# Optimization experiments

Measured on AMD Instinct MI355X. Metric: run time of the kernel, lower is better.

The kernel has to match this reference:

```python
import jax, jax.numpy as jnp
import numpy as np

N_NODES = 100000
N_EDGES = 1600000
IN_F, HID_F, OUT_F = 128, 128, 64
BN_EPS = 1e-5


def _glorot(key, shape):
    lim = np.sqrt(6.0 / (shape[0] + shape[1]))
    return jax.random.uniform(key, shape, jnp.float32, -lim, lim)


def setup_inputs() -> dict:
    key = jax.random.key(0)
    ks = jax.random.split(key, 12)
    x = jax.random.normal(ks[0], (N_NODES, IN_F), jnp.float32)
    src = jax.random.randint(ks[1], (N_EDGES,), 0, N_NODES, jnp.int64)
    dst = jax.random.randint(ks[2], (N_EDGES,), 0, N_NODES, jnp.int64)
    dims = [(IN_F, HID_F), (HID_F, HID_F), (HID_F, OUT_F)]
    inp = {"x": x, "src": src, "dst": dst}
    for i, (di, do) in enumerate(dims):
        inp[f"w_self{i}"] = _glorot(ks[3 + 2 * i], (di, do))
        inp[f"w_neigh{i}"] = _glorot(ks[4 + 2 * i], (di, do))
        inp[f"b{i}"] = jnp.zeros((do,), jnp.float32)
    for i in range(2):  # BatchNorm1d(hid) after first two convs
        inp[f"gamma{i}"] = jnp.ones((HID_F,), jnp.float32)
        inp[f"beta{i}"] = jnp.zeros((HID_F,), jnp.float32)
    return inp


def _sage_conv(h, src, dst, w_self, w_neigh, b):
    # mean aggregation over incoming edges: gather src feats, segment-sum by dst
    deg = jax.ops.segment_sum(jnp.ones((src.shape[0],), h.dtype), dst, num_segments=N_NODES)
    agg = jax.ops.segment_sum(h[src], dst, num_segments=N_NODES)
    agg = agg / jnp.maximum(deg, 1.0)[:, None]
    return h @ w_self + agg @ w_neigh + b


def _batchnorm(h, gamma, beta):
    mu = jnp.mean(h, axis=0)
    var = jnp.var(h, axis=0)
    return (h - mu) * jax.lax.rsqrt(var + BN_EPS) * gamma + beta


def reference(x, src, dst, w_self0, w_neigh0, b0, gamma0, beta0,
              w_self1, w_neigh1, b1, gamma1, beta1, w_self2, w_neigh2, b2):
    h = _sage_conv(x, src, dst, w_self0, w_neigh0, b0)
    h = jax.nn.relu(_batchnorm(h, gamma0, beta0))
    h = _sage_conv(h, src, dst, w_self1, w_neigh1, b1)
    h = jax.nn.relu(_batchnorm(h, gamma1, beta1))
    h = _sage_conv(h, src, dst, w_self2, w_neigh2, b2)
    return jax.nn.log_softmax(h, axis=-1)
```

## Files before the change

### kernel.cpp

```cpp
#include <hip/hip_runtime.h>
#include <hip/hip_bf16.h>

typedef unsigned short u16;
typedef unsigned char  u8;
typedef unsigned int   u32;
typedef __attribute__((ext_vector_type(8))) short short8;
typedef __attribute__((ext_vector_type(4))) float floatx4;
typedef __attribute__((ext_vector_type(2))) float floatx2;

__device__ __forceinline__ float bits2f(u32 v){ float f; __builtin_memcpy(&f, &v, 4); return f; }
__device__ __forceinline__ u16 f2bf(float f){
    __hip_bfloat16 h = __float2bfloat16(f);
    u16 u; __builtin_memcpy(&u, &h, 2); return u;
}

__device__ __forceinline__ void gload_lds16(const void* g, void* l){
    __builtin_amdgcn_global_load_lds(
        (const __attribute__((address_space(1))) unsigned char*)g,
        (__attribute__((address_space(3))) unsigned char*)l, 16, 0, 0);
}


__global__ __launch_bounds__(256) void cvt_kernel(const float* __restrict__ in,
                                                  u16* __restrict__ out,
                                                  u32* __restrict__ out8, int total4){
    int i = blockIdx.x * 256 + threadIdx.x;
    if (i >= total4) return;
    float4 v = ((const float4*)in)[i];
    uint2 o;
    o.x = (u32)f2bf(v.x) | ((u32)f2bf(v.y) << 16);
    o.y = (u32)f2bf(v.z) | ((u32)f2bf(v.w) << 16);
    ((uint2*)out)[i] = o;
    u32 p8 = (u32)__builtin_amdgcn_cvt_pk_fp8_f32(v.x, v.y, 0, false);
    p8     = (u32)__builtin_amdgcn_cvt_pk_fp8_f32(v.z, v.w, (int)p8, true);
    out8[i] = p8;
}


__global__ __launch_bounds__(256) void cvt8a_kernel(const u16* __restrict__ in,
                                                    const float* __restrict__ cs,
                                                    uint2* __restrict__ out8, int total8){
    int i = blockIdx.x * 256 + threadIdx.x;
    if (i >= total8) return;
    const int c0 = (i & 15) * 8;
    uint4 v = ((const uint4*)in)[i];
    u32 w[4] = {v.x, v.y, v.z, v.w};
    float f[8];
    #pragma unroll
    for (int j = 0; j < 4; ++j){
        f[2*j]   = bits2f(w[j] << 16);
        f[2*j+1] = bits2f(w[j] & 0xffff0000u);
    }
    #pragma unroll
    for (int j = 0; j < 8; ++j)
        f[j] = fmaxf(fmaf(f[j], cs[256 + c0 + j], cs[384 + c0 + j]), 0.f);
    u32 lo = (u32)__builtin_amdgcn_cvt_pk_fp8_f32(f[0], f[1], 0, false);
    lo     = (u32)__builtin_amdgcn_cvt_pk_fp8_f32(f[2], f[3], (int)lo, true);
    u32 hi = (u32)__builtin_amdgcn_cvt_pk_fp8_f32(f[4], f[5], 0, false);
    hi     = (u32)__builtin_amdgcn_cvt_pk_fp8_f32(f[6], f[7], (int)hi, true);
    uint2 o; o.x = lo; o.y = hi;
    out8[i] = o;
}


__global__ __launch_bounds__(256) void bhist_kernel(const int* __restrict__ dst,
                                                    int* __restrict__ gbcnt, int E){
    __shared__ int bc[256];
    const int t = threadIdx.x;
    bc[t] = 0;
    __syncthreads();
    const int tile0 = blockIdx.x * 8192;
    const int cnt = min(8192, E - tile0);
    for (int j = t; j < cnt; j += 256) atomicAdd(&bc[dst[tile0 + j] >> 9], 1);
    __syncthreads();
    if (bc[t] > 0) atomicAdd(&gbcnt[t], bc[t]);
}

__global__ __launch_bounds__(256) void bscan_kernel(const int* __restrict__ gbcnt,
                                                    int* __restrict__ bbase,
                                                    int* __restrict__ bcur, int nbuk){
    __shared__ int ws[4];
    const int t = threadIdx.x, lane = t & 63, wv = t >> 6;
    int v = (t < nbuk) ? gbcnt[t] : 0;
    int s = v;
    for (int off = 1; off < 64; off <<= 1){
        int n = __shfl_up(s, off);
        if (lane >= off) s += n;
    }
    if (lane == 63) ws[wv] = s;
    __syncthreads();
    int woff = 0;
    for (int w = 0; w < wv; ++w) woff += ws[w];
    int excl = s + woff - v;
    if (t < nbuk){ bbase[t] = excl; bcur[t] = excl; }
}

#define BIN_TILE 8192
__global__ __launch_bounds__(256) void bin_kernel(const int* __restrict__ src,
                                                  const int* __restrict__ dst,
                                                  int* __restrict__ bcur,
                                                  u32* __restrict__ pairs, int E, int nbuk){
    __shared__ u32 hcnt[256], hexcl[256], hoff[256];
    __shared__ int gbase[256];
    __shared__ u32 stage[BIN_TILE];
    __shared__ unsigned char bkt[BIN_TILE];
    const int t = threadIdx.x;
    const int tile0 = blockIdx.x * BIN_TILE;
    const int cntE = min(BIN_TILE, E - tile0);

    hcnt[t] = 0;
    __syncthreads();
    for (int j = t; j < cntE; j += 256){
        int d = dst[tile0 + j];
        atomicAdd(&hcnt[d >> 9], 1u);
    }
    __syncthreads();
    if (t < 64){
        u32 a0 = hcnt[4*t], a1 = hcnt[4*t+1], a2 = hcnt[4*t+2], a3 = hcnt[4*t+3];
        u32 lsum = a0 + a1 + a2 + a3;
        u32 s = lsum;
        for (int off = 1; off < 64; off <<= 1){
            u32 n = __shfl_up(s, off);
            if (t >= off) s += n;
        }
        u32 base = s - lsum;
        hexcl[4*t]   = base;
        hexcl[4*t+1] = base + a0;
        hexcl[4*t+2] = base + a0 + a1;
        hexcl[4*t+3] = base + a0 + a1 + a2;
        hoff[4*t]   = base;
        hoff[4*t+1] = base + a0;
        hoff[4*t+2] = base + a0 + a1;
        hoff[4*t+3] = base + a0 + a1 + a2;
    }
    __syncthreads();
    if (t < nbuk && hcnt[t] > 0) gbase[t] = atomicAdd(&bcur[t], (int)hcnt[t]);
    for (int j = t; j < cntE; j += 256){
        int d = dst[tile0 + j];
        int s = src[tile0 + j];
        int b = d >> 9;
        u32 p = atomicAdd(&hoff[b], 1u);
        stage[p] = ((u32)s << 9) | (u32)(d & 511);
        bkt[p] = (unsigned char)b;
    }
    __syncthreads();
    for (int j = t; j < cntE; j += 256){
        int b = bkt[j];
        pairs[gbase[b] + (int)((u32)j - hexcl[b])] = stage[j];
    }
}

__global__ __launch_bounds__(256) void sort2_kernel(const u32* __restrict__ pairs,
                                                    const int* __restrict__ bbase,
                                                    int* __restrict__ indptr,
                                                    float* __restrict__ invdeg,
                                                    int* __restrict__ esrc,
                                                    int M, int E, int nbuk){
    __shared__ int ndeg[512];
    __shared__ int cur[512];
    __shared__ int wsI[4];
    const int b = blockIdx.x;
    const int node0 = b * 512;
    const int lo = bbase[b];
    const int hi = (b + 1 < nbuk) ? bbase[b + 1] : E;
    const int t = threadIdx.x, lane = t & 63, wv = t >> 6;

    ndeg[t] = 0; ndeg[t + 256] = 0;
    __syncthreads();
    for (int i = lo + t; i < hi; i += 256) atomicAdd(&ndeg[pairs[i] & 511], 1);
    __syncthreads();

    const int d0 = ndeg[2*t], d1 = ndeg[2*t + 1];
    const int p = d0 + d1;
    int s = p;
    for (int off = 1; off < 64; off <<= 1){
        int n = __shfl_up(s, off);
        if (lane >= off) s += n;
    }
    if (lane == 63) wsI[wv] = s;
    __syncthreads();
    int woff = 0;
    for (int w = 0; w < wv; ++w) woff += wsI[w];
    const int incl = s + woff;
    const int excl0 = incl - p;
    const int excl1 = excl0 + d0;

    const int n0 = node0 + 2*t, n1 = node0 + 2*t + 1;
    if (n0 < M){
        indptr[n0 + 1] = lo + excl0 + d0;
        invdeg[n0] = 1.0f / (float)max(d0, 1);
        cur[2*t] = lo + excl0;
    }
    if (n1 < M){
        indptr[n1 + 1] = lo + excl1 + d1;
        invdeg[n1] = 1.0f / (float)max(d1, 1);
        cur[2*t + 1] = lo + excl1;
    }
    if (b == 0 && t == 0) indptr[0] = 0;
    __syncthreads();
    for (int i = lo + t; i < hi; i += 256){
        u32 v = pairs[i];
        int pos = atomicAdd(&cur[v & 511], 1);
        esrc[pos] = (int)(v >> 9);
    }
}


__global__ void pack_kernel(const float* __restrict__ wself, const float* __restrict__ wneigh,
                            u16* __restrict__ bp, int N){
    int i = blockIdx.x * 256 + threadIdx.x;
    if (i >= N * 256) return;
    int n = i >> 8, k = i & 255;
    float v = (k < 128) ? wself[k * N + n] : wneigh[(k - 128) * N + n];
    bp[i] = f2bf(v);
}


__global__ __launch_bounds__(256) void agg_kernel(const u8* __restrict__ h8,
                                                  const int* __restrict__ indptr,
                                                  const int* __restrict__ esrc,
                                                  const float* __restrict__ invdeg,
                                                  u16* __restrict__ agg, int M){
    const int l8 = threadIdx.x & 7;
    const int n = (blockIdx.x * 256 + threadIdx.x) >> 3;
    if (n >= M) return;
    const int beg = indptr[n];
    const int end = indptr[n + 1];
    const float fs = invdeg[n];

    floatx2 acc[8];
    #pragma unroll
    for (int i = 0; i < 8; ++i){ acc[i].x = 0.f; acc[i].y = 0.f; }

    const u8* hb = h8 + l8 * 16;

    auto accum = [&](uint4 v){
        u32 w[4] = {v.x, v.y, v.z, v.w};
        #pragma unroll
        for (int j = 0; j < 4; ++j){
            acc[2*j]   += __builtin_amdgcn_cvt_pk_f32_fp8(w[j], false);
            acc[2*j+1] += __builtin_amdgcn_cvt_pk_f32_fp8(w[j], true);
        }
    };

    int e = beg;
    for (; e + 4 <= end; e += 4){
        const int i0 = esrc[e];
        const int i1 = esrc[e + 1];
        const int i2 = esrc[e + 2];
        const int i3 = esrc[e + 3];
        uint4 v0 = *(const uint4*)(hb + (size_t)i0 * 128);
        uint4 v1 = *(const uint4*)(hb + (size_t)i1 * 128);
        uint4 v2 = *(const uint4*)(hb + (size_t)i2 * 128);
        uint4 v3 = *(const uint4*)(hb + (size_t)i3 * 128);
        accum(v0); accum(v1); accum(v2); accum(v3);
    }
    for (; e < end; ++e){
        const int i0 = esrc[e];
        uint4 v0 = *(const uint4*)(hb + (size_t)i0 * 128);
        accum(v0);
    }

    u32 o[8];
    #pragma unroll
    for (int k = 0; k < 8; ++k)
        o[k] = (u32)f2bf(acc[k].x * fs) | ((u32)f2bf(acc[k].y * fs) << 16);
    uint4 w0 = {o[0], o[1], o[2], o[3]};
    uint4 w1 = {o[4], o[5], o[6], o[7]};
    *(uint4*)(agg + (size_t)n * 128 + l8 * 16)     = w0;
    *(uint4*)(agg + (size_t)n * 128 + l8 * 16 + 8) = w1;
}


template<int NTW, bool STATS, bool AFFA>
__global__ __launch_bounds__(256, 4) void gemm3_kernel(const u16* __restrict__ hA,
                                                       const u16* __restrict__ aggA,
                                                       const u16* __restrict__ Bp,
                                                       const float* __restrict__ bias,
                                                       const float* __restrict__ cs,
                                                       void* __restrict__ outPre,
                                                       float* __restrict__ partials,
                                                       int M, int T, int GBs){
    constexpr int N = NTW * 64;
    __shared__ __align__(16) u16 Abuf[3][4096];
    __shared__ __align__(16) char cbuf[2][4352];
    __shared__ float s_sc[128], s_sh[128];

    const int wave = threadIdx.x >> 6;
    const int lane = threadIdx.x & 63;
    const int m15 = lane & 15;
    const int quad = lane >> 4;
    const int colbase = wave * (NTW * 16);

    if (AFFA && threadIdx.x < 128){
        s_sc[threadIdx.x] = cs[256 + threadIdx.x];
        s_sh[threadIdx.x] = cs[384 + threadIdx.x];
    }
    __syncthreads();

    short8 breg[NTW][8];
    float bv[NTW];
    #pragma unroll
    for (int nt = 0; nt < NTW; ++nt){
        bv[nt] = bias[colbase + nt * 16 + m15];
        #pragma unroll
        for (int k0 = 0; k0 < 8; ++k0)
            breg[nt][k0] = *(const short8*)(Bp + (size_t)(colbase + nt * 16 + m15) * 256 + k0 * 32 + quad * 8);
    }

    float sS[NTW], sQ[NTW];
    #pragma unroll
    for (int nt = 0; nt < NTW; ++nt){ sS[nt] = 0.f; sQ[nt] = 0.f; }

    auto stage = [&](int bufIdx, int tile){
        const int srow = lane & 15, squad = lane >> 4;
        int arow = tile * 16 + srow;
        if (arow >= M) arow = M - 1;
        #pragma unroll
        for (int h = 0; h < 2; ++h){
            const int k0 = wave * 2 + h;
            const u16* base = (k0 < 4) ? hA : aggA;
            const u16* g = base + (size_t)arow * 128 + (k0 & 3) * 32 + squad * 8;
            gload_lds16(g, &Abuf[bufIdx][k0 * 512]);
        }
    };

    const int t0 = blockIdx.x;
    const int nIter = (T - 1 - t0) / GBs + 1;

    stage(0, t0);
    if (nIter > 1) stage(1, t0 + GBs);

    int t = t0;
    for (int it = 0; it < nIter; ++it){
        const int cur = it % 3;
        if (it + 2 < nIter) stage((it + 2) % 3, t + 2 * GBs);

        const int ahead = min(nIter - 1 - it, 2);
        if (ahead >= 2)      asm volatile("s_waitcnt vmcnt(4)" ::: "memory");
        else if (ahead == 1) asm volatile("s_waitcnt vmcnt(2)" ::: "memory");
        else                 asm volatile("s_waitcnt vmcnt(0)" ::: "memory");
        __builtin_amdgcn_s_barrier();
        __builtin_amdgcn_sched_barrier(0);

        floatx4 acc[NTW];
        #pragma unroll
        for (int nt = 0; nt < NTW; ++nt) acc[nt] = 0.0f;
        #pragma unroll
        for (int k0 = 0; k0 < 8; ++k0){
            short8 a = *(const short8*)&Abuf[cur][k0 * 512 + quad * 128 + m15 * 8];
            if (AFFA && k0 < 4){
                const int cb = k0 * 32 + quad * 8;
                #pragma unroll
                for (int j = 0; j < 8; ++j){
                    float f = bits2f(((u32)(u16)a[j]) << 16);
                    f = fmaxf(fmaf(f, s_sc[cb + j], s_sh[cb + j]), 0.f);
                    a[j] = (short)f2bf(f);
                }
            }
            #pragma unroll
            for (int nt = 0; nt < NTW; ++nt)
                acc[nt] = __builtin_amdgcn_mfma_f32_16x16x32_bf16(a, breg[nt][k0], acc[nt], 0, 0, 0);
        }

        char* cb = &cbuf[it & 1][0];
        const int r0 = quad * 4;
        #pragma unroll
        for (int nt = 0; nt < NTW; ++nt){
            const int col = colbase + nt * 16 + m15;
            #pragma unroll
            for (int r = 0; r < 4; ++r){
                float v = acc[nt][r] + bv[nt];
                if (STATS){
                    int row = t * 16 + r0 + r;
                    if (row < M){
                        sS[nt] += v;
                        sQ[nt] = fmaf(v, v, sQ[nt]);
                    }
                    ((u16*)cb)[(r0 + r) * 136 + col] = f2bf(v);
                } else {
                    ((float*)cb)[(r0 + r) * 68 + col] = v;
                }
            }
        }
        asm volatile("s_waitcnt lgkmcnt(0)" ::: "memory");
        __builtin_amdgcn_s_barrier();
        __builtin_amdgcn_sched_barrier(0);

        const int srow = threadIdx.x >> 4, seg = threadIdx.x & 15;
        const int grow = t * 16 + srow;
        if (grow < M){
            if (STATS){
                uint4 w = *(const uint4*)((const u16*)cb + srow * 136 + seg * 8);
                *(uint4*)((u16*)outPre + (size_t)grow * N + seg * 8) = w;
            } else {
                float4 w = *(const float4*)((const float*)cb + srow * 68 + seg * 4);
                *(float4*)((float*)outPre + (size_t)grow * N + seg * 4) = w;
            }
        }
        t += GBs;
    }

    if (STATS){
        #pragma unroll
        for (int nt = 0; nt < NTW; ++nt){
            float s = sS[nt], q = sQ[nt];
            s += __shfl_xor(s, 16);  s += __shfl_xor(s, 32);
            q += __shfl_xor(q, 16);  q += __shfl_xor(q, 32);
            if (quad == 0){
                const int c = colbase + nt * 16 + m15;
                partials[(size_t)blockIdx.x * 256 + c]       = s;
                partials[(size_t)blockIdx.x * 256 + 128 + c] = q;
            }
        }
    }
}


__global__ __launch_bounds__(256) void bnred_kernel(const float* __restrict__ partials,
                                                    float* __restrict__ cs, int nblk){
    const int t = threadIdx.x;
    float s = 0.f;
    for (int b = blockIdx.x; b < nblk; b += (int)gridDim.x)
        s += partials[(size_t)b * 256 + t];
    atomicAdd(&cs[t], s);
}

__global__ void bnfin_kernel(float* __restrict__ cs, const float* __restrict__ gamma,
                             const float* __restrict__ beta, float invM){
    int c = threadIdx.x;
    float mu  = cs[c] * invM;
    float var = fmaxf(cs[128 + c] * invM - mu * mu, 0.0f);
    float sc  = gamma[c] * rsqrtf(var + 1e-5f);
    cs[256 + c] = sc;
    cs[384 + c] = beta[c] - mu * sc;
}


__global__ __launch_bounds__(256) void lsm_kernel(const float* __restrict__ pre,
                                                  float* __restrict__ out, int M){
    const int wave = threadIdx.x >> 6;
    const int lane = threadIdx.x & 63;
    const int row = blockIdx.x * 4 + wave;
    if (row >= M) return;
    float v = pre[(size_t)row * 64 + lane];
    float m = v;
    #pragma unroll
    for (int o = 32; o; o >>= 1) m = fmaxf(m, __shfl_xor(m, o));
    float e = __expf(v - m);
    float s = e;
    #pragma unroll
    for (int o = 32; o; o >>= 1) s += __shfl_xor(s, o);
    out[(size_t)row * 64 + lane] = v - m - __logf(s);
}


extern "C" void kernel_launch(void* const* d_in, const int* in_sizes, int n_in,
                              void* d_out, int out_size, void* d_ws, size_t ws_size,
                              hipStream_t stream) {
    const float* x   = (const float*)d_in[0];
    const int*   src = (const int*)d_in[1];
    const int*   dst = (const int*)d_in[2];
    const float* wself[3]  = {(const float*)d_in[3], (const float*)d_in[6], (const float*)d_in[9]};
    const float* wneigh[3] = {(const float*)d_in[4], (const float*)d_in[7], (const float*)d_in[10]};
    const float* bias[3]   = {(const float*)d_in[5], (const float*)d_in[8], (const float*)d_in[11]};
    const float* gamma[2]  = {(const float*)d_in[12], (const float*)d_in[14]};
    const float* beta[2]   = {(const float*)d_in[13], (const float*)d_in[15]};

    const int M = in_sizes[0] / 128;
    const int E = in_sizes[1];
    const int NBUK = (M + 511) / 512;
    const int T = (M + 15) / 16;
    const int GB = 1024;

    char* ws = (char*)d_ws;
    size_t off = 0;
    auto alloc = [&](size_t bytes) -> void* {
        void* p = ws + off;
        off = (off + bytes + 511) & ~(size_t)511;
        return p;
    };
    int*   gbcnt  = (int*)alloc(256 * 4);
    int*   bbase  = (int*)alloc(256 * 4);
    int*   bcur   = (int*)alloc(256 * 4);
    int*   indptr = (int*)alloc((size_t)(M + 1) * 4);
    u32*   pairs  = (u32*)alloc((size_t)E * 4);
    int*   esrc   = (int*)alloc((size_t)E * 4);
    float* invdeg = (float*)alloc((size_t)M * 4);
    u16* bpack0 = (u16*)alloc(128 * 256 * 2);
    u16* bpack1 = (u16*)alloc(128 * 256 * 2);
    u16* bpack2 = (u16*)alloc(64 * 256 * 2);
    float* colstat0 = (float*)alloc(512 * 4);
    float* colstat1 = (float*)alloc(512 * 4);
    float* partials = (float*)alloc((size_t)GB * 256 * 4);
    u16*   hbuf   = (u16*)alloc((size_t)M * 128 * 2);
    u16*   aggbuf = (u16*)alloc((size_t)M * 128 * 2);
    u16*   preA   = (u16*)alloc((size_t)M * 128 * 2);
    u16*   preB   = (u16*)alloc((size_t)M * 128 * 2);
    float* preF   = (float*)alloc((size_t)M * 64 * 4);
    u8*    x8     = (u8*)alloc((size_t)M * 128);
    u8*    preA8  = (u8*)alloc((size_t)M * 128);
    u8*    preB8  = (u8*)alloc((size_t)M * 128);

    hipMemsetAsync(gbcnt, 0, 256 * 4, stream);
    bhist_kernel<<<(E + 8191) / 8192, 256, 0, stream>>>(dst, gbcnt, E);
    bscan_kernel<<<1, 256, 0, stream>>>(gbcnt, bbase, bcur, NBUK);
    bin_kernel<<<(E + BIN_TILE - 1) / BIN_TILE, 256, 0, stream>>>(src, dst, bcur, pairs, E, NBUK);
    sort2_kernel<<<NBUK, 256, 0, stream>>>(pairs, bbase, indptr, invdeg, esrc, M, E, NBUK);

    cvt_kernel<<<((M * 32) + 255) / 256, 256, 0, stream>>>(x, hbuf, (u32*)x8, M * 32);
    pack_kernel<<<(128 * 256 + 255) / 256, 256, 0, stream>>>(wself[0], wneigh[0], bpack0, 128);
    pack_kernel<<<(128 * 256 + 255) / 256, 256, 0, stream>>>(wself[1], wneigh[1], bpack1, 128);
    pack_kernel<<<(64 * 256 + 255) / 256, 256, 0, stream>>>(wself[2], wneigh[2], bpack2, 64);

    agg_kernel<<<(M + 31) / 32, 256, 0, stream>>>(x8, indptr, esrc, invdeg, aggbuf, M);
    gemm3_kernel<2, true, false><<<GB, 256, 0, stream>>>(hbuf, aggbuf, bpack0, bias[0], nullptr,
                                                         preA, partials, M, T, GB);
    hipMemsetAsync(colstat0, 0, 256 * 4, stream);
    bnred_kernel<<<32, 256, 0, stream>>>(partials, colstat0, GB);
    bnfin_kernel<<<1, 128, 0, stream>>>(colstat0, gamma[0], beta[0], 1.0f / (float)M);
    cvt8a_kernel<<<((M * 16) + 255) / 256, 256, 0, stream>>>(preA, colstat0, (uint2*)preA8, M * 16);

    agg_kernel<<<(M + 31) / 32, 256, 0, stream>>>(preA8, indptr, esrc, invdeg, aggbuf, M);
    gemm3_kernel<2, true, true><<<GB, 256, 0, stream>>>(preA, aggbuf, bpack1, bias[1], colstat0,
                                                        preB, partials, M, T, GB);
    hipMemsetAsync(colstat1, 0, 256 * 4, stream);
    bnred_kernel<<<32, 256, 0, stream>>>(partials, colstat1, GB);
    bnfin_kernel<<<1, 128, 0, stream>>>(colstat1, gamma[1], beta[1], 1.0f / (float)M);
    cvt8a_kernel<<<((M * 16) + 255) / 256, 256, 0, stream>>>(preB, colstat1, (uint2*)preB8, M * 16);

    agg_kernel<<<(M + 31) / 32, 256, 0, stream>>>(preB8, indptr, esrc, invdeg, aggbuf, M);
    gemm3_kernel<1, false, true><<<GB, 256, 0, stream>>>(preB, aggbuf, bpack2, bias[2], colstat1,
                                                         preF, partials, M, T, GB);
    lsm_kernel<<<(M + 3) / 4, 256, 0, stream>>>(preF, (float*)d_out, M);
}
```

Baseline: 427.9 us.

## Fuse log-softmax into final GEMM, merge BN reduce/finalize, batch weight packing

Log-softmax now runs in the last GEMM's epilogue using 16-lane shuffles over each 64-wide row, so the fp32 intermediate is never written and read back and one kernel launch goes away. The two-step BN reduction (memset, atomic reduce, finalize) becomes one kernel that reads column-major partials with one wave per column. The three weight pack launches become one. Together these cut launch count and a round trip of an M×64 fp32 buffer, at the cost of extra transcendental work in the GEMM epilogue.

```diff
diff --git a/kernel.cpp b/kernel.cpp
--- a/kernel.cpp
+++ b/kernel.cpp
@@ -206,12 +206,18 @@
 }
 
 
-__global__ void pack_kernel(const float* __restrict__ wself, const float* __restrict__ wneigh,
-                            u16* __restrict__ bp, int N){
+__global__ __launch_bounds__(256) void pack3_kernel(const float* __restrict__ w0s, const float* __restrict__ w0n,
+                                                    const float* __restrict__ w1s, const float* __restrict__ w1n,
+                                                    const float* __restrict__ w2s, const float* __restrict__ w2n,
+                                                    u16* __restrict__ bp0, u16* __restrict__ bp1,
+                                                    u16* __restrict__ bp2){
     int i = blockIdx.x * 256 + threadIdx.x;
-    if (i >= N * 256) return;
+    const float *ws, *wn; u16* bp; int N;
+    if (i < 32768){ ws = w0s; wn = w0n; bp = bp0; N = 128; }
+    else if (i < 65536){ i -= 32768; ws = w1s; wn = w1n; bp = bp1; N = 128; }
+    else { i -= 65536; ws = w2s; wn = w2n; bp = bp2; N = 64; }
     int n = i >> 8, k = i & 255;
-    float v = (k < 128) ? wself[k * N + n] : wneigh[(k - 128) * N + n];
+    float v = (k < 128) ? ws[k * N + n] : wn[(k - 128) * N + n];
     bp[i] = f2bf(v);
 }
 
@@ -272,7 +278,7 @@
 }
 
 
-template<int NTW, bool STATS, bool AFFA>
+template<int NTW, bool STATS, bool AFFA, bool LSM>
 __global__ __launch_bounds__(256, 4) void gemm3_kernel(const u16* __restrict__ hA,
                                                        const u16* __restrict__ aggA,
                                                        const u16* __restrict__ Bp,
@@ -389,7 +395,25 @@
 
         const int srow = threadIdx.x >> 4, seg = threadIdx.x & 15;
         const int grow = t * 16 + srow;
-        if (grow < M){
+        if (LSM){
+            float4 w = *(const float4*)((const float*)cb + srow * 68 + seg * 4);
+            float m = fmaxf(fmaxf(w.x, w.y), fmaxf(w.z, w.w));
+            m = fmaxf(m, __shfl_xor(m, 1));
+            m = fmaxf(m, __shfl_xor(m, 2));
+            m = fmaxf(m, __shfl_xor(m, 4));
+            m = fmaxf(m, __shfl_xor(m, 8));
+            float e = __expf(w.x - m) + __expf(w.y - m) + __expf(w.z - m) + __expf(w.w - m);
+            e += __shfl_xor(e, 1);
+            e += __shfl_xor(e, 2);
+            e += __shfl_xor(e, 4);
+            e += __shfl_xor(e, 8);
+            float lg = m + __logf(e);
+            if (grow < M){
+                float4 o;
+                o.x = w.x - lg; o.y = w.y - lg; o.z = w.z - lg; o.w = w.w - lg;
+                *(float4*)((float*)outPre + (size_t)grow * 64 + seg * 4) = o;
+            }
+        } else if (grow < M){
             if (STATS){
                 uint4 w = *(const uint4*)((const u16*)cb + srow * 136 + seg * 8);
                 *(uint4*)((u16*)outPre + (size_t)grow * N + seg * 8) = w;
@@ -409,49 +433,34 @@
             q += __shfl_xor(q, 16);  q += __shfl_xor(q, 32);
             if (quad == 0){
                 const int c = colbase + nt * 16 + m15;
-                partials[(size_t)blockIdx.x * 256 + c]       = s;
-                partials[(size_t)blockIdx.x * 256 + 128 + c] = q;
+                partials[(size_t)c * GBs + blockIdx.x]         = s;
+                partials[(size_t)(128 + c) * GBs + blockIdx.x] = q;
             }
         }
     }
 }
 
 
-__global__ __launch_bounds__(256) void bnred_kernel(const float* __restrict__ partials,
-                                                    float* __restrict__ cs, int nblk){
-    const int t = threadIdx.x;
-    float s = 0.f;
-    for (int b = blockIdx.x; b < nblk; b += (int)gridDim.x)
-        s += partials[(size_t)b * 256 + t];
-    atomicAdd(&cs[t], s);
-}
-
-__global__ void bnfin_kernel(float* __restrict__ cs, const float* __restrict__ gamma,
-                             const float* __restrict__ beta, float invM){
-    int c = threadIdx.x;
-    float mu  = cs[c] * invM;
-    float var = fmaxf(cs[128 + c] * invM - mu * mu, 0.0f);
-    float sc  = gamma[c] * rsqrtf(var + 1e-5f);
-    cs[256 + c] = sc;
-    cs[384 + c] = beta[c] - mu * sc;
-}
-
-
-__global__ __launch_bounds__(256) void lsm_kernel(const float* __restrict__ pre,
-                                                  float* __restrict__ out, int M){
-    const int wave = threadIdx.x >> 6;
-    const int lane = threadIdx.x & 63;
-    const int row = blockIdx.x * 4 + wave;
-    if (row >= M) return;
-    float v = pre[(size_t)row * 64 + lane];
-    float m = v;
-    #pragma unroll
-    for (int o = 32; o; o >>= 1) m = fmaxf(m, __shfl_xor(m, o));
-    float e = __expf(v - m);
-    float s = e;
-    #pragma unroll
-    for (int o = 32; o; o >>= 1) s += __shfl_xor(s, o);
-    out[(size_t)row * 64 + lane] = v - m - __logf(s);
+__global__ __launch_bounds__(256) void bnstat_kernel(const float* __restrict__ partials,
+                                                     float* __restrict__ cs,
+                                                     const float* __restrict__ gamma,
+                                                     const float* __restrict__ beta,
+                                                     float invM, int GB){
+    const int wv = threadIdx.x >> 6, lane = threadIdx.x & 63;
+    const int c = blockIdx.x * 4 + wv;
+    float s = 0.f, q = 0.f;
+    const float* ps = partials + (size_t)c * GB;
+    const float* pq = partials + (size_t)(128 + c) * GB;
+    for (int k = lane; k < GB; k += 64){ s += ps[k]; q += pq[k]; }
+    #pragma unroll
+    for (int o = 32; o; o >>= 1){ s += __shfl_xor(s, o); q += __shfl_xor(q, o); }
+    if (lane == 0){
+        float mu  = s * invM;
+        float var = fmaxf(q * invM - mu * mu, 0.f);
+        float sc  = gamma[c] * rsqrtf(var + 1e-5f);
+        cs[256 + c] = sc;
+        cs[384 + c] = beta[c] - mu * sc;
+    }
 }
 
 
@@ -497,7 +506,6 @@
     u16*   aggbuf = (u16*)alloc((size_t)M * 128 * 2);
     u16*   preA   = (u16*)alloc((size_t)M * 128 * 2);
     u16*   preB   = (u16*)alloc((size_t)M * 128 * 2);
-    float* preF   = (float*)alloc((size_t)M * 64 * 4);
     u8*    x8     = (u8*)alloc((size_t)M * 128);
     u8*    preA8  = (u8*)alloc((size_t)M * 128);
     u8*    preB8  = (u8*)alloc((size_t)M * 128);
@@ -509,28 +517,22 @@
     sort2_kernel<<<NBUK, 256, 0, stream>>>(pairs, bbase, indptr, invdeg, esrc, M, E, NBUK);
 
     cvt_kernel<<<((M * 32) + 255) / 256, 256, 0, stream>>>(x, hbuf, (u32*)x8, M * 32);
-    pack_kernel<<<(128 * 256 + 255) / 256, 256, 0, stream>>>(wself[0], wneigh[0], bpack0, 128);
-    pack_kernel<<<(128 * 256 + 255) / 256, 256, 0, stream>>>(wself[1], wneigh[1], bpack1, 128);
-    pack_kernel<<<(64 * 256 + 255) / 256, 256, 0, stream>>>(wself[2], wneigh[2], bpack2, 64);
+    pack3_kernel<<<320, 256, 0, stream>>>(wself[0], wneigh[0], wself[1], wneigh[1],
+                                          wself[2], wneigh[2], bpack0, bpack1, bpack2);
 
     agg_kernel<<<(M + 31) / 32, 256, 0, stream>>>(x8, indptr, esrc, invdeg, aggbuf, M);
-    gemm3_kernel<2, true, false><<<GB, 256, 0, stream>>>(hbuf, aggbuf, bpack0, bias[0], nullptr,
-                                                         preA, partials, M, T, GB);
-    hipMemsetAsync(colstat0, 0, 256 * 4, stream);
-    bnred_kernel<<<32, 256, 0, stream>>>(partials, colstat0, GB);
-    bnfin_kernel<<<1, 128, 0, stream>>>(colstat0, gamma[0], beta[0], 1.0f / (float)M);
+    gemm3_kernel<2, true, false, false><<<GB, 256, 0, stream>>>(hbuf, aggbuf, bpack0, bias[0], nullptr,
+                                                                preA, partials, M, T, GB);
+    bnstat_kernel<<<32, 256, 0, stream>>>(partials, colstat0, gamma[0], beta[0], 1.0f / (float)M, GB);
     cvt8a_kernel<<<((M * 16) + 255) / 256, 256, 0, stream>>>(preA, colstat0, (uint2*)preA8, M * 16);
 
     agg_kernel<<<(M + 31) / 32, 256, 0, stream>>>(preA8, indptr, esrc, invdeg, aggbuf, M);
-    gemm3_kernel<2, true, true><<<GB, 256, 0, stream>>>(preA, aggbuf, bpack1, bias[1], colstat0,
-                                                        preB, partials, M, T, GB);
-    hipMemsetAsync(colstat1, 0, 256 * 4, stream);
-    bnred_kernel<<<32, 256, 0, stream>>>(partials, colstat1, GB);
-    bnfin_kernel<<<1, 128, 0, stream>>>(colstat1, gamma[1], beta[1], 1.0f / (float)M);
+    gemm3_kernel<2, true, true, false><<<GB, 256, 0, stream>>>(preA, aggbuf, bpack1, bias[1], colstat0,
+                                                               preB, partials, M, T, GB);
+    bnstat_kernel<<<32, 256, 0, stream>>>(partials, colstat1, gamma[1], beta[1], 1.0f / (float)M, GB);
     cvt8a_kernel<<<((M * 16) + 255) / 256, 256, 0, stream>>>(preB, colstat1, (uint2*)preB8, M * 16);
 
     agg_kernel<<<(M + 31) / 32, 256, 0, stream>>>(preB8, indptr, esrc, invdeg, aggbuf, M);
-    gemm3_kernel<1, false, true><<<GB, 256, 0, stream>>>(preB, aggbuf, bpack2, bias[2], colstat1,
-                                                         preF, partials, M, T, GB);
-    lsm_kernel<<<(M + 3) / 4, 256, 0, stream>>>(preF, (float*)d_out, M);
-}
+    gemm3_kernel<1, false, true, true><<<GB, 256, 0, stream>>>(preB, aggbuf, bpack2, bias[2], colstat1,
+                                                               d_out, partials, M, T, GB);
+}
```

Result: faster. 402.0 us (-6.1%).
